# Performance work log

Measured on AMD Instinct MI355X. Metric: run time of the kernel, lower is better.

## Reference

```python
import jax, jax.numpy as jnp
import numpy as np

N, K, P_DIM, HID, NCLS = 20000, 16, 63, 32 + 0, 32
HID = 128
IN_DIM = P_DIM + 1


def setup_inputs() -> dict:
    key = jax.random.key(0)
    ks = iter(jax.random.split(key, 64))

    def nrm(shape, s=0.1):
        return jax.random.normal(next(ks), shape, jnp.float32) * s

    inp = {
        "p": nrm((N, P_DIM), 1.0),
        "neigh_idx": jax.random.randint(next(ks), (N, K), 0, N, dtype=jnp.int32),
    }
    dims = [(IN_DIM, HID), (HID, HID), (HID, NCLS)]
    for l, (din, dout) in enumerate(dims):
        inp[f"l{l}_Wih"] = nrm((4 * din, din))
        inp[f"l{l}_Whh"] = nrm((4 * din, din))
        inp[f"l{l}_bih"] = jnp.zeros((4 * din,), jnp.float32)
        inp[f"l{l}_bhh"] = jnp.zeros((4 * din,), jnp.float32)
        inp[f"l{l}_Wself"] = nrm((dout, din))
        inp[f"l{l}_Wneigh"] = nrm((dout, din))
        inp[f"l{l}_b"] = jnp.zeros((dout,), jnp.float32)
    return inp


def _lstm_agg(feat, neigh_idx, Wih, Whh, bih, bhh):
    # Per-node LSTM over the K in-neighbor features (DGL _lstm_reducer).
    n, h_dim = feat.shape[0], Whh.shape[1]
    bias = bih + bhh

    def step(carry, idx_t):
        h, c = carry
        x = feat[idx_t]                                   # [N, Din] gather (step t message)
        g = x @ Wih.T + h @ Whh.T + bias                  # [N, 4H]
        i, f, gg, o = jnp.split(g, 4, axis=-1)            # torch LSTM gate order i,f,g,o
        c = jax.nn.sigmoid(f) * c + jax.nn.sigmoid(i) * jnp.tanh(gg)
        h = jax.nn.sigmoid(o) * jnp.tanh(c)
        return (h, c), None

    init = (jnp.zeros((n, h_dim), feat.dtype), jnp.zeros((n, h_dim), feat.dtype))
    (h, _), _ = jax.lax.scan(step, init, neigh_idx.T)     # scan over K neighbor slots
    return h                                              # final hidden state = neigh feat


def _forward(p, neigh_idx, *params):
    # features = cat(in_degree/N, p); fixed-degree graph -> in_degree == K
    deg = jnp.full((p.shape[0], 1), K / N, p.dtype)
    feat = jnp.concatenate([deg, p], axis=1)
    layers = [params[7 * l: 7 * (l + 1)] for l in range(3)]
    for l, (Wih, Whh, bih, bhh, Wself, Wneigh, b) in enumerate(layers):
        neigh = _lstm_agg(feat, neigh_idx, Wih, Whh, bih, bhh)
        feat = feat @ Wself.T + neigh @ Wneigh.T + b      # fc_self + fc_neigh + bias
        if l < 2:
            feat = jax.nn.relu(feat)
    return feat


def reference(p, neigh_idx,
              l0_Wih, l0_Whh, l0_bih, l0_bhh, l0_Wself, l0_Wneigh, l0_b,
              l1_Wih, l1_Whh, l1_bih, l1_bhh, l1_Wself, l1_Wneigh, l1_b,
              l2_Wih, l2_Whh, l2_bih, l2_bhh, l2_Wself, l2_Wneigh, l2_b):
    return _forward(p, neigh_idx,
                    l0_Wih, l0_Whh, l0_bih, l0_bhh, l0_Wself, l0_Wneigh, l0_b,
                    l1_Wih, l1_Whh, l1_bih, l1_bhh, l1_Wself, l1_Wneigh, l1_b,
                    l2_Wih, l2_Whh, l2_bih, l2_bhh, l2_Wself, l2_Wneigh, l2_b)
```

## Files before the change

kernel.cpp:

```cpp
#include <hip/hip_runtime.h>
#include <hip/hip_bf16.h>
#include <stdint.h>


#define N_NODES 20000
#define KNE 16

typedef __bf16 bf16x8 __attribute__((ext_vector_type(8)));
typedef float f32x4 __attribute__((ext_vector_type(4)));

__device__ __forceinline__ bf16x8 ldb8(const __hip_bfloat16* p) {
  uint4 u = *reinterpret_cast<const uint4*>(p);
  return __builtin_bit_cast(bf16x8, u);
}
__device__ __forceinline__ float b2f_lo(uint32_t u) {
  return __builtin_bit_cast(float, u << 16);
}
__device__ __forceinline__ float b2f_hi(uint32_t u) {
  return __builtin_bit_cast(float, u & 0xffff0000u);
}
__device__ __forceinline__ float sigf(float x) {
  float t = __builtin_amdgcn_exp2f(-1.442695041f * x);
  return __builtin_amdgcn_rcpf(1.f + t);
}
__device__ __forceinline__ float tanhf_(float x) {
  float t = __builtin_amdgcn_exp2f(2.885390082f * x);
  return 1.f - 2.f * __builtin_amdgcn_rcpf(t + 1.f);
}

__global__ void build_feat0(const float* __restrict__ p,
                            __hip_bfloat16* __restrict__ f0) {
  int i = blockIdx.x * 256 + threadIdx.x;
  if (i >= N_NODES * 64) return;
  int n = i >> 6, c = i & 63;
  float v = (c == 0) ? ((float)KNE / (float)N_NODES) : p[n * 63 + c - 1];
  f0[i] = __float2bfloat16(v);
}

__global__ void cvt4(const float* __restrict__ s0, int n0,
                     const float* __restrict__ s1, int n1,
                     const float* __restrict__ s2, int n2,
                     const float* __restrict__ s3, int n3,
                     __hip_bfloat16* __restrict__ d0,
                     __hip_bfloat16* __restrict__ d1,
                     __hip_bfloat16* __restrict__ d2,
                     __hip_bfloat16* __restrict__ d3) {
  int i = blockIdx.x * 256 + threadIdx.x;
  if (i < n0) { d0[i] = __float2bfloat16(s0[i]); return; }
  i -= n0;
  if (i < n1) { d1[i] = __float2bfloat16(s1[i]); return; }
  i -= n1;
  if (i < n2) { d2[i] = __float2bfloat16(s2[i]); return; }
  i -= n2;
  if (i < n3) d3[i] = __float2bfloat16(s3[i]);
}

template <int DIN, int DOUT>
__global__ __launch_bounds__(256, 2) void proj_kern(
    const __hip_bfloat16* __restrict__ feat,
    const __hip_bfloat16* __restrict__ Wih,
    const float* __restrict__ bih,
    const float* __restrict__ bhh,
    const __hip_bfloat16* __restrict__ Wself,
    const float* __restrict__ bvec,
    __hip_bfloat16* __restrict__ P, float* __restrict__ S) {
  constexpr int KB = DIN / 32;
  constexpr int CTP = 4 * DIN / 16;
  constexpr int CTS = DOUT / 16;
  const int n0 = blockIdx.x * 32;
  const int tid = threadIdx.x;
  const int wv = tid >> 6;
  const int lane = tid & 63;
  const int quad = lane >> 4;
  const int c16 = lane & 15;

  bf16x8 afr[2][KB];
#pragma unroll
  for (int rt = 0; rt < 2; ++rt)
#pragma unroll
    for (int kb = 0; kb < KB; ++kb)
      afr[rt][kb] =
          ldb8(feat + (size_t)(n0 + rt * 16 + c16) * DIN + kb * 32 + quad * 8);

  const f32x4 zz = {0.f, 0.f, 0.f, 0.f};
  for (int ct = wv; ct < CTP + CTS; ct += 4) {
    f32x4 a0 = zz, a1 = zz;
    const __hip_bfloat16* W;
    int row;
    if (ct < CTP) { W = Wih; row = ct * 16 + c16; }
    else          { W = Wself; row = (ct - CTP) * 16 + c16; }
#pragma unroll
    for (int kb = 0; kb < KB; ++kb) {
      bf16x8 b = ldb8(W + (size_t)row * DIN + kb * 32 + quad * 8);
      a0 = __builtin_amdgcn_mfma_f32_16x16x32_bf16(afr[0][kb], b, a0, 0, 0, 0);
      a1 = __builtin_amdgcn_mfma_f32_16x16x32_bf16(afr[1][kb], b, a1, 0, 0, 0);
    }
    if (ct < CTP) {
      int c = ct * 16 + c16;
      int gg = c / DIN, cc = c % DIN;
      float bias = bih[c] + bhh[c];
#pragma unroll
      for (int r = 0; r < 4; ++r) {
        P[(size_t)(n0 + quad * 4 + r) * (4 * DIN) + cc * 4 + gg] =
            __float2bfloat16(a0[r] + bias);
        P[(size_t)(n0 + 16 + quad * 4 + r) * (4 * DIN) + cc * 4 + gg] =
            __float2bfloat16(a1[r] + bias);
      }
    } else {
      int c = (ct - CTP) * 16 + c16;
      float bias = bvec[c];
#pragma unroll
      for (int r = 0; r < 4; ++r) {
        S[(size_t)(n0 + quad * 4 + r) * DOUT + c] = a0[r] + bias;
        S[(size_t)(n0 + 16 + quad * 4 + r) * DOUT + c] = a1[r] + bias;
      }
    }
  }
}

template <int DIN, int DOUT, bool RELU, typename OutT>
__global__ __launch_bounds__(256, 2) void lstm_fc_kern(
    const __hip_bfloat16* __restrict__ P,
    const float* __restrict__ S,
    const __hip_bfloat16* __restrict__ Whh,
    const __hip_bfloat16* __restrict__ Wng,
    const int* __restrict__ nidx,
    OutT* __restrict__ outp) {
  constexpr int CW = DIN / 4;
  constexpr int JJ = CW / 16;
  constexpr int KB = DIN / 32;
  constexpr int HS = DIN + 8;

  __shared__ __align__(16) __hip_bfloat16 hl[2][16 * HS];
  __shared__ int idxl[16 * KNE];

  const int n0 = blockIdx.x * 16;
  const int tid = threadIdx.x;
  const int wv = tid >> 6;
  const int lane = tid & 63;
  const int quad = lane >> 4;
  const int c16 = lane & 15;

  for (int i = tid; i < 16 * KNE; i += 256) idxl[i] = nidx[n0 * KNE + i];

  bf16x8 Bp[4][JJ][KB];
#pragma unroll
  for (int g = 0; g < 4; ++g)
#pragma unroll
    for (int jj = 0; jj < JJ; ++jj)
#pragma unroll
      for (int kb = 0; kb < KB; ++kb)
        Bp[g][jj][kb] =
            ldb8(Whh + (size_t)(g * DIN + wv * CW + jj * 16 + c16) * DIN +
                 kb * 32 + quad * 8);

  float cst[4][JJ];
#pragma unroll
  for (int r = 0; r < 4; ++r)
#pragma unroll
    for (int jj = 0; jj < JJ; ++jj) cst[r][jj] = 0.f;

  uint2 pf[4][JJ];
  auto loadpf = [&](int t) {
#pragma unroll
    for (int r = 0; r < 4; ++r) {
      int src = idxl[(quad * 4 + r) * KNE + t];
      const uint2* bp =
          reinterpret_cast<const uint2*>(P + (size_t)src * (4 * DIN));
#pragma unroll
      for (int jj = 0; jj < JJ; ++jj) pf[r][jj] = bp[wv * CW + jj * 16 + c16];
    }
  };

  auto gates = [&](int buf, const f32x4 (&ag)[4][JJ]) {
#pragma unroll
    for (int jj = 0; jj < JJ; ++jj)
#pragma unroll
      for (int r = 0; r < 4; ++r) {
        float vi = ag[0][jj][r] + b2f_lo(pf[r][jj].x);
        float vf = ag[1][jj][r] + b2f_hi(pf[r][jj].x);
        float vg = ag[2][jj][r] + b2f_lo(pf[r][jj].y);
        float vo = ag[3][jj][r] + b2f_hi(pf[r][jj].y);
        float cc = sigf(vf) * cst[r][jj] + sigf(vi) * tanhf_(vg);
        cst[r][jj] = cc;
        hl[buf][(quad * 4 + r) * HS + wv * CW + jj * 16 + c16] =
            __float2bfloat16(sigf(vo) * tanhf_(cc));
      }
  };

  const f32x4 zz = {0.f, 0.f, 0.f, 0.f};

  __syncthreads();
  loadpf(0);
  {
    f32x4 ag[4][JJ];
#pragma unroll
    for (int g = 0; g < 4; ++g)
#pragma unroll
      for (int jj = 0; jj < JJ; ++jj) ag[g][jj] = zz;
    gates(0, ag);
  }

  for (int t = 1; t < KNE; ++t) {
    __syncthreads();
    loadpf(t);
    const int pb = (t - 1) & 1;
    bf16x8 Af[KB];
#pragma unroll
    for (int kb = 0; kb < KB; ++kb)
      Af[kb] = ldb8(&hl[pb][c16 * HS + kb * 32 + quad * 8]);
    f32x4 ag[4][JJ];
#pragma unroll
    for (int g = 0; g < 4; ++g)
#pragma unroll
      for (int jj = 0; jj < JJ; ++jj) ag[g][jj] = zz;
#pragma unroll
    for (int kb = 0; kb < KB; ++kb)
#pragma unroll
      for (int g = 0; g < 4; ++g)
#pragma unroll
        for (int jj = 0; jj < JJ; ++jj)
          ag[g][jj] = __builtin_amdgcn_mfma_f32_16x16x32_bf16(
              Af[kb], Bp[g][jj][kb], ag[g][jj], 0, 0, 0);
    gates(t & 1, ag);
  }

  __syncthreads();
  bf16x8 Hf[KB];
#pragma unroll
  for (int kb = 0; kb < KB; ++kb)
    Hf[kb] = ldb8(&hl[1][c16 * HS + kb * 32 + quad * 8]);
  for (int ct = wv; ct < DOUT / 16; ct += 4) {
    f32x4 a = zz;
#pragma unroll
    for (int kb = 0; kb < KB; ++kb) {
      bf16x8 b = ldb8(Wng + (size_t)(ct * 16 + c16) * DIN + kb * 32 + quad * 8);
      a = __builtin_amdgcn_mfma_f32_16x16x32_bf16(Hf[kb], b, a, 0, 0, 0);
    }
#pragma unroll
    for (int r = 0; r < 4; ++r) {
      int n = n0 + quad * 4 + r;
      int col = ct * 16 + c16;
      float v = a[r] + S[(size_t)n * DOUT + col];
      if (RELU) v = fmaxf(v, 0.f);
      if constexpr (sizeof(OutT) == 2)
        outp[(size_t)n * DOUT + col] = __float2bfloat16(v);
      else
        outp[(size_t)n * DOUT + col] = v;
    }
  }
}

extern "C" void kernel_launch(void* const* d_in, const int* in_sizes, int n_in,
                              void* d_out, int out_size, void* d_ws,
                              size_t ws_size, hipStream_t stream) {
  (void)in_sizes; (void)n_in; (void)out_size; (void)ws_size;
  const float* p = (const float*)d_in[0];
  const int* nidx = (const int*)d_in[1];
  const float* L[3][7];
  for (int l = 0; l < 3; ++l)
    for (int j = 0; j < 7; ++j)
      L[l][j] = (const float*)d_in[2 + 7 * l + j];

  char* w = (char*)d_ws;
  __hip_bfloat16* feat0 = (__hip_bfloat16*)(w);
  __hip_bfloat16* feat1 = (__hip_bfloat16*)(w + 2560000);
  __hip_bfloat16* feat2 = (__hip_bfloat16*)(w + 7680000);
  __hip_bfloat16* Pb    = (__hip_bfloat16*)(w + 12800000);
  float*          Sb    = (float*)(w + 33280000);
  __hip_bfloat16* wb    = (__hip_bfloat16*)(w + 43520000);

  const int din_[3] = {64, 128, 128}, dout_[3] = {128, 128, 32};
  __hip_bfloat16 *Wih_b[3], *Whh_b[3], *Wself_b[3], *Wng_b[3];
  size_t off = 0;
  for (int l = 0; l < 3; ++l) {
    int din = din_[l], dout = dout_[l];
    Wih_b[l] = wb + off;   off += (size_t)4 * din * din;
    Whh_b[l] = wb + off;   off += (size_t)4 * din * din;
    Wself_b[l] = wb + off; off += (size_t)dout * din;
    Wng_b[l] = wb + off;   off += (size_t)dout * din;
  }
  for (int l = 0; l < 3; ++l) {
    int din = din_[l], dout = dout_[l];
    int n0 = 4 * din * din, n2 = dout * din;
    int tot = 2 * n0 + 2 * n2;
    cvt4<<<(tot + 255) / 256, 256, 0, stream>>>(
        L[l][0], n0, L[l][1], n0, L[l][4], n2, L[l][5], n2,
        Wih_b[l], Whh_b[l], Wself_b[l], Wng_b[l]);
  }

  build_feat0<<<(N_NODES * 64 + 255) / 256, 256, 0, stream>>>(p, feat0);

  proj_kern<64, 128><<<N_NODES / 32, 256, 0, stream>>>(
      feat0, Wih_b[0], L[0][2], L[0][3], Wself_b[0], L[0][6], Pb, Sb);
  lstm_fc_kern<64, 128, true, __hip_bfloat16>
      <<<N_NODES / 16, 256, 0, stream>>>(Pb, Sb, Whh_b[0], Wng_b[0], nidx,
                                         feat1);

  proj_kern<128, 128><<<N_NODES / 32, 256, 0, stream>>>(
      feat1, Wih_b[1], L[1][2], L[1][3], Wself_b[1], L[1][6], Pb, Sb);
  lstm_fc_kern<128, 128, true, __hip_bfloat16>
      <<<N_NODES / 16, 256, 0, stream>>>(Pb, Sb, Whh_b[1], Wng_b[1], nidx,
                                         feat2);

  proj_kern<128, 32><<<N_NODES / 32, 256, 0, stream>>>(
      feat2, Wih_b[2], L[2][2], L[2][3], Wself_b[2], L[2][6], Pb, Sb);
  lstm_fc_kern<128, 32, false, float>
      <<<N_NODES / 16, 256, 0, stream>>>(Pb, Sb, Whh_b[2], Wng_b[2], nidx,
                                         (float*)d_out);
}
```

Baseline: 396.5 us.

## Scale LSTM block to DIN/16 waves and double-buffer neighbor gate prefetch

The LSTM kernel now launches DIN/16 waves per block, so the DIN=128 layers use 512 threads and each wave owns a single 16-column slice of every gate. This cuts the per-thread Whh register footprint and the MFMA chain length per wave, trading it for more waves per barrier. The projected-gate gather is also double-buffered: the next timestep's neighbor rows are fetched one step ahead, overlapping global loads with the recurrent MFMA and gate math. The first layer keeps 256 threads because DIN=64 gives 4 waves.

```diff
diff --git a/kernel.cpp b/kernel.cpp
--- a/kernel.cpp
+++ b/kernel.cpp
@@ -119,15 +119,14 @@
 }
 
 template <int DIN, int DOUT, bool RELU, typename OutT>
-__global__ __launch_bounds__(256, 2) void lstm_fc_kern(
+__global__ __launch_bounds__((DIN / 16) * 64, 2) void lstm_fc_kern(
     const __hip_bfloat16* __restrict__ P,
     const float* __restrict__ S,
     const __hip_bfloat16* __restrict__ Whh,
     const __hip_bfloat16* __restrict__ Wng,
     const int* __restrict__ nidx,
     OutT* __restrict__ outp) {
-  constexpr int CW = DIN / 4;
-  constexpr int JJ = CW / 16;
+  constexpr int W = DIN / 16;
   constexpr int KB = DIN / 32;
   constexpr int HS = DIN + 8;
 
@@ -140,89 +139,74 @@
   const int lane = tid & 63;
   const int quad = lane >> 4;
   const int c16 = lane & 15;
-
-  for (int i = tid; i < 16 * KNE; i += 256) idxl[i] = nidx[n0 * KNE + i];
-
-  bf16x8 Bp[4][JJ][KB];
-#pragma unroll
-  for (int g = 0; g < 4; ++g)
-#pragma unroll
-    for (int jj = 0; jj < JJ; ++jj)
-#pragma unroll
-      for (int kb = 0; kb < KB; ++kb)
-        Bp[g][jj][kb] =
-            ldb8(Whh + (size_t)(g * DIN + wv * CW + jj * 16 + c16) * DIN +
-                 kb * 32 + quad * 8);
-
-  float cst[4][JJ];
-#pragma unroll
-  for (int r = 0; r < 4; ++r)
-#pragma unroll
-    for (int jj = 0; jj < JJ; ++jj) cst[r][jj] = 0.f;
-
-  uint2 pf[4][JJ];
-  auto loadpf = [&](int t) {
+  const int col = wv * 16 + c16;
+
+  for (int i = tid; i < 16 * KNE; i += W * 64) idxl[i] = nidx[n0 * KNE + i];
+  __syncthreads();
+
+  uint2 pf[2][4];
+  auto loadpf = [&](int t, int b) {
 #pragma unroll
     for (int r = 0; r < 4; ++r) {
       int src = idxl[(quad * 4 + r) * KNE + t];
-      const uint2* bp =
-          reinterpret_cast<const uint2*>(P + (size_t)src * (4 * DIN));
-#pragma unroll
-      for (int jj = 0; jj < JJ; ++jj) pf[r][jj] = bp[wv * CW + jj * 16 + c16];
+      pf[b][r] =
+          reinterpret_cast<const uint2*>(P + (size_t)src * (4 * DIN))[col];
     }
   };
 
-  auto gates = [&](int buf, const f32x4 (&ag)[4][JJ]) {
-#pragma unroll
-    for (int jj = 0; jj < JJ; ++jj)
-#pragma unroll
-      for (int r = 0; r < 4; ++r) {
-        float vi = ag[0][jj][r] + b2f_lo(pf[r][jj].x);
-        float vf = ag[1][jj][r] + b2f_hi(pf[r][jj].x);
-        float vg = ag[2][jj][r] + b2f_lo(pf[r][jj].y);
-        float vo = ag[3][jj][r] + b2f_hi(pf[r][jj].y);
-        float cc = sigf(vf) * cst[r][jj] + sigf(vi) * tanhf_(vg);
-        cst[r][jj] = cc;
-        hl[buf][(quad * 4 + r) * HS + wv * CW + jj * 16 + c16] =
-            __float2bfloat16(sigf(vo) * tanhf_(cc));
-      }
+  loadpf(0, 0);
+
+  bf16x8 Bp[4][KB];
+#pragma unroll
+  for (int g = 0; g < 4; ++g)
+#pragma unroll
+    for (int kb = 0; kb < KB; ++kb)
+      Bp[g][kb] =
+          ldb8(Whh + (size_t)(g * DIN + col) * DIN + kb * 32 + quad * 8);
+
+  loadpf(1, 1);
+
+  float cst[4];
+#pragma unroll
+  for (int r = 0; r < 4; ++r) cst[r] = 0.f;
+
+  auto gates = [&](int hb, int b, const f32x4 (&ag)[4]) {
+#pragma unroll
+    for (int r = 0; r < 4; ++r) {
+      float vi = ag[0][r] + b2f_lo(pf[b][r].x);
+      float vf = ag[1][r] + b2f_hi(pf[b][r].x);
+      float vg = ag[2][r] + b2f_lo(pf[b][r].y);
+      float vo = ag[3][r] + b2f_hi(pf[b][r].y);
+      float cc = sigf(vf) * cst[r] + sigf(vi) * tanhf_(vg);
+      cst[r] = cc;
+      hl[hb][(quad * 4 + r) * HS + col] =
+          __float2bfloat16(sigf(vo) * tanhf_(cc));
+    }
   };
 
   const f32x4 zz = {0.f, 0.f, 0.f, 0.f};
 
-  __syncthreads();
-  loadpf(0);
   {
-    f32x4 ag[4][JJ];
-#pragma unroll
-    for (int g = 0; g < 4; ++g)
-#pragma unroll
-      for (int jj = 0; jj < JJ; ++jj) ag[g][jj] = zz;
-    gates(0, ag);
+    f32x4 ag[4] = {zz, zz, zz, zz};
+    gates(0, 0, ag);
   }
 
   for (int t = 1; t < KNE; ++t) {
     __syncthreads();
-    loadpf(t);
+    if (t + 1 < KNE) loadpf(t + 1, (t + 1) & 1);
     const int pb = (t - 1) & 1;
     bf16x8 Af[KB];
 #pragma unroll
     for (int kb = 0; kb < KB; ++kb)
       Af[kb] = ldb8(&hl[pb][c16 * HS + kb * 32 + quad * 8]);
-    f32x4 ag[4][JJ];
-#pragma unroll
-    for (int g = 0; g < 4; ++g)
-#pragma unroll
-      for (int jj = 0; jj < JJ; ++jj) ag[g][jj] = zz;
+    f32x4 ag[4] = {zz, zz, zz, zz};
 #pragma unroll
     for (int kb = 0; kb < KB; ++kb)
 #pragma unroll
       for (int g = 0; g < 4; ++g)
-#pragma unroll
-        for (int jj = 0; jj < JJ; ++jj)
-          ag[g][jj] = __builtin_amdgcn_mfma_f32_16x16x32_bf16(
-              Af[kb], Bp[g][jj][kb], ag[g][jj], 0, 0, 0);
-    gates(t & 1, ag);
+        ag[g] = __builtin_amdgcn_mfma_f32_16x16x32_bf16(Af[kb], Bp[g][kb],
+                                                        ag[g], 0, 0, 0);
+    gates(t & 1, t & 1, ag);
   }
 
   __syncthreads();
@@ -230,7 +214,7 @@
 #pragma unroll
   for (int kb = 0; kb < KB; ++kb)
     Hf[kb] = ldb8(&hl[1][c16 * HS + kb * 32 + quad * 8]);
-  for (int ct = wv; ct < DOUT / 16; ct += 4) {
+  for (int ct = wv; ct < DOUT / 16; ct += W) {
     f32x4 a = zz;
 #pragma unroll
     for (int kb = 0; kb < KB; ++kb) {
@@ -240,13 +224,13 @@
 #pragma unroll
     for (int r = 0; r < 4; ++r) {
       int n = n0 + quad * 4 + r;
-      int col = ct * 16 + c16;
-      float v = a[r] + S[(size_t)n * DOUT + col];
+      int c = ct * 16 + c16;
+      float v = a[r] + S[(size_t)n * DOUT + c];
       if (RELU) v = fmaxf(v, 0.f);
       if constexpr (sizeof(OutT) == 2)
-        outp[(size_t)n * DOUT + col] = __float2bfloat16(v);
+        outp[(size_t)n * DOUT + c] = __float2bfloat16(v);
       else
-        outp[(size_t)n * DOUT + col] = v;
+        outp[(size_t)n * DOUT + c] = v;
     }
   }
 }
@@ -300,12 +284,12 @@
   proj_kern<128, 128><<<N_NODES / 32, 256, 0, stream>>>(
       feat1, Wih_b[1], L[1][2], L[1][3], Wself_b[1], L[1][6], Pb, Sb);
   lstm_fc_kern<128, 128, true, __hip_bfloat16>
-      <<<N_NODES / 16, 256, 0, stream>>>(Pb, Sb, Whh_b[1], Wng_b[1], nidx,
+      <<<N_NODES / 16, 512, 0, stream>>>(Pb, Sb, Whh_b[1], Wng_b[1], nidx,
                                          feat2);
 
   proj_kern<128, 32><<<N_NODES / 32, 256, 0, stream>>>(
       feat2, Wih_b[2], L[2][2], L[2][3], Wself_b[2], L[2][6], Pb, Sb);
   lstm_fc_kern<128, 32, false, float>
-      <<<N_NODES / 16, 256, 0, stream>>>(Pb, Sb, Whh_b[2], Wng_b[2], nidx,
+      <<<N_NODES / 16, 512, 0, stream>>>(Pb, Sb, Whh_b[2], Wng_b[2], nidx,
                                          (float*)d_out);
 }
```

Result: slower. 489.5 us (+23.4%).
